# Optimization experiments

Measured on AMD Instinct MI355X. Metric: run time of the kernel, lower is better.

The kernel has to match this reference:

```python
import jax, jax.numpy as jnp
import numpy as np

COMMITMENT_COST = 0.25


def setup_inputs() -> dict:
    key = jax.random.key(0)
    k1, k2 = jax.random.split(key)
    B, S, D, K = 8, 4096, 256, 1024
    inputs = jax.random.normal(k1, (B, S, D), dtype=jnp.float32)
    attention_mask = jnp.ones((B, S), dtype=jnp.float32)
    codebook = jax.random.normal(k2, (K, D), dtype=jnp.float32)
    return {"inputs": inputs, "attention_mask": attention_mask, "codebook": codebook}


def reference(inputs, attention_mask, codebook):
    # Inference-mode forward of VectorQuantizer (no EMA update / init / revival).
    B, S, D = inputs.shape
    z = inputs.astype(jnp.float32).reshape(-1, D)          # (N, D)
    m = attention_mask.reshape(-1).astype(jnp.float32)     # (N,)

    cb = codebook.astype(jnp.float32)                      # (K, D)
    # squared L2 distances: ||z||^2 - 2 z e^T + ||e||^2
    dist = (jnp.sum(z * z, axis=-1, keepdims=True)
            - 2.0 * jnp.matmul(z, cb.T)
            + jnp.sum(cb * cb, axis=-1)[None, :])          # (N, K)
    idx = jnp.argmin(dist, axis=-1)                        # (N,)
    q = cb[idx]                                            # (N, D) codebook lookup

    n_valid = jnp.sum(m)
    # mse over valid tokens (elementwise mean, matching F.mse_loss on flat_valid)
    diff = z - jax.lax.stop_gradient(q)
    commitment = jnp.sum(m[:, None] * diff * diff) / (n_valid * D)
    vq_loss = COMMITMENT_COST * commitment

    # straight-through estimator; invalid positions zeroed (as in torch scatter)
    q_ste = z + jax.lax.stop_gradient(q - z)
    quantized = (q_ste * m[:, None]).reshape(B, S, D)
    indices = jnp.where(m > 0, idx, 0).reshape(B, S)
    return quantized, vq_loss, indices
```

## Files before the change

### kernel.cpp

```cpp
#include <hip/hip_runtime.h>
#include <cstdint>

typedef short bf16x8 __attribute__((ext_vector_type(8)));
typedef float f32x4  __attribute__((ext_vector_type(4)));

#define TOK    64
#define PITCH  264
#define HROWS  (64 * PITCH)
#define MAXC   32

__device__ __forceinline__ unsigned short f2bf(float f) {
  unsigned u = __float_as_uint(f);
  return (unsigned short)((u + 0x7FFFu + ((u >> 16) & 1u)) >> 16);
}
__device__ __forceinline__ uint4 pack8(float4 a, float4 b) {
  uint4 u;
  u.x = (unsigned)f2bf(a.x) | ((unsigned)f2bf(a.y) << 16);
  u.y = (unsigned)f2bf(a.z) | ((unsigned)f2bf(a.w) << 16);
  u.z = (unsigned)f2bf(b.x) | ((unsigned)f2bf(b.y) << 16);
  u.w = (unsigned)f2bf(b.z) | ((unsigned)f2bf(b.w) << 16);
  return u;
}

__global__ __launch_bounds__(256) void vq_prep(const float* __restrict__ cb,
                                               unsigned short* __restrict__ cb_bf,
                                               float* __restrict__ ee,
                                               float* __restrict__ acc2,
                                               int* __restrict__ done_ctr, int K) {
  if (blockIdx.x == 0 && threadIdx.x == 0) {
    acc2[0] = 0.f; acc2[1] = 0.f; *done_ctr = 0;
  }
  int wave = threadIdx.x >> 6, lane = threadIdx.x & 63;
  int k = blockIdx.x * 4 + wave;
  if (k >= K) return;
  float4 v = *reinterpret_cast<const float4*>(cb + (size_t)k * 256 + lane * 4);
  float s = v.x * v.x + v.y * v.y + v.z * v.z + v.w * v.w;
  #pragma unroll
  for (int off = 32; off; off >>= 1) s += __shfl_down(s, off, 64);
  ushort4 b;
  b.x = f2bf(v.x); b.y = f2bf(v.y); b.z = f2bf(v.z); b.w = f2bf(v.w);
  *reinterpret_cast<ushort4*>(cb_bf + (size_t)k * 256 + lane * 4) = b;
  if (lane == 0) ee[k] = s;
}

__global__ __launch_bounds__(256, 2) void vq_main(
    const float* __restrict__ z, const float* __restrict__ cb,
    const unsigned short* __restrict__ cb_bf, const float* __restrict__ ee,
    const float* __restrict__ mask,
    float* __restrict__ out_q, float* __restrict__ out_idx_f,
    float* __restrict__ out_loss, float* __restrict__ acc2,
    int* __restrict__ done_ctr, int nblocks, int K) {
  __shared__ __align__(16) unsigned short buf[128 * PITCH];
  __shared__ float ee_lds[1024];
  __shared__ float znorm[TOK];
  __shared__ int   ccnt[TOK];
  __shared__ unsigned short cand[TOK * MAXC];
  __shared__ float red[8];
  __shared__ bool  last;

  const int t = threadIdx.x;
  const int n0 = blockIdx.x * TOK;
  const int q16 = t & 15;

  ee_lds[t]       = ee[t];
  ee_lds[t + 256] = ee[t + 256];
  ee_lds[t + 512] = ee[t + 512];
  ee_lds[t + 768] = ee[t + 768];
  if (t < TOK) ccnt[t] = 0;

  #pragma unroll
  for (int pass = 0; pass < 4; ++pass) {
    int row = pass * 16 + (t >> 4);
    const float* zr = z + (size_t)(n0 + row) * 256;
    float ssq = 0.f;
    #pragma unroll
    for (int j = 0; j < 2; ++j) {
      float4 a = *reinterpret_cast<const float4*>(zr + q16 * 8 + j * 128);
      float4 b = *reinterpret_cast<const float4*>(zr + q16 * 8 + j * 128 + 4);
      ssq += a.x*a.x + a.y*a.y + a.z*a.z + a.w*a.w
           + b.x*b.x + b.y*b.y + b.z*b.z + b.w*b.w;
      *reinterpret_cast<uint4*>(&buf[row * PITCH + q16 * 8 + j * 128]) = pack8(a, b);
    }
    #pragma unroll
    for (int off = 1; off < 16; off <<= 1) ssq += __shfl_xor(ssq, off, 64);
    if (q16 == 0) znorm[row] = sqrtf(ssq);
  }
  __syncthreads();

  const int wv = t >> 6, lane = t & 63;
  const int p = wv & 1, kh = wv >> 1;
  const int quad = lane >> 4, l15 = lane & 15;
  bf16x8 afrag[2][8];
  float  znreg[2][4];
  #pragma unroll
  for (int s = 0; s < 2; ++s) {
    const unsigned short* za = &buf[(p * 32 + s * 16 + l15) * PITCH + quad * 8];
    #pragma unroll
    for (int kk = 0; kk < 8; ++kk)
      afrag[s][kk] = *reinterpret_cast<const bf16x8*>(za + kk * 32);
    #pragma unroll
    for (int r = 0; r < 4; ++r)
      znreg[s][r] = znorm[p * 32 + s * 16 + quad * 4 + r];
  }
  __syncthreads();

  float amin[2][4];
  #pragma unroll
  for (int s = 0; s < 2; ++s)
    #pragma unroll
    for (int r = 0; r < 4; ++r) amin[s][r] = 3.4e38f;

  const int tq = (p << 6) | lane;
  const int sq16 = tq & 15, srow = tq >> 4;
  unsigned short* qbuf = &buf[kh * HROWS];

  for (int lc = 0; lc < 8; ++lc) {
    const int kbase = kh * 512 + lc * 64;
    #pragma unroll
    for (int pass = 0; pass < 8; ++pass) {
      int row = pass * 8 + srow;
      const unsigned short* src = cb_bf + (size_t)(kbase + row) * 256;
      #pragma unroll
      for (int j = 0; j < 2; ++j) {
        uint4 v = *reinterpret_cast<const uint4*>(src + sq16 * 8 + j * 128);
        *reinterpret_cast<uint4*>(&qbuf[row * PITCH + sq16 * 8 + j * 128]) = v;
      }
    }
    __syncthreads();

    f32x4 acc[2][4];
    #pragma unroll
    for (int s = 0; s < 2; ++s)
      #pragma unroll
      for (int ct = 0; ct < 4; ++ct) acc[s][ct] = (f32x4){0.f, 0.f, 0.f, 0.f};
    #pragma unroll
    for (int kk = 0; kk < 8; ++kk) {
      bf16x8 b0 = *reinterpret_cast<const bf16x8*>(&qbuf[(l15)      * PITCH + quad * 8 + kk * 32]);
      bf16x8 b1 = *reinterpret_cast<const bf16x8*>(&qbuf[(16 + l15) * PITCH + quad * 8 + kk * 32]);
      bf16x8 b2 = *reinterpret_cast<const bf16x8*>(&qbuf[(32 + l15) * PITCH + quad * 8 + kk * 32]);
      bf16x8 b3 = *reinterpret_cast<const bf16x8*>(&qbuf[(48 + l15) * PITCH + quad * 8 + kk * 32]);
      acc[0][0] = __builtin_amdgcn_mfma_f32_16x16x32_bf16(afrag[0][kk], b0, acc[0][0], 0, 0, 0);
      acc[1][0] = __builtin_amdgcn_mfma_f32_16x16x32_bf16(afrag[1][kk], b0, acc[1][0], 0, 0, 0);
      acc[0][1] = __builtin_amdgcn_mfma_f32_16x16x32_bf16(afrag[0][kk], b1, acc[0][1], 0, 0, 0);
      acc[1][1] = __builtin_amdgcn_mfma_f32_16x16x32_bf16(afrag[1][kk], b1, acc[1][1], 0, 0, 0);
      acc[0][2] = __builtin_amdgcn_mfma_f32_16x16x32_bf16(afrag[0][kk], b2, acc[0][2], 0, 0, 0);
      acc[1][2] = __builtin_amdgcn_mfma_f32_16x16x32_bf16(afrag[1][kk], b2, acc[1][2], 0, 0, 0);
      acc[0][3] = __builtin_amdgcn_mfma_f32_16x16x32_bf16(afrag[0][kk], b3, acc[0][3], 0, 0, 0);
      acc[1][3] = __builtin_amdgcn_mfma_f32_16x16x32_bf16(afrag[1][kk], b3, acc[1][3], 0, 0, 0);
    }

    float e0 = ee_lds[kbase + l15],      e1 = ee_lds[kbase + 16 + l15];
    float e2 = ee_lds[kbase + 32 + l15], e3 = ee_lds[kbase + 48 + l15];
    float en0 = sqrtf(e0), en1 = sqrtf(e1), en2 = sqrtf(e2), en3 = sqrtf(e3);
    #pragma unroll
    for (int s = 0; s < 2; ++s) {
      #pragma unroll
      for (int r = 0; r < 4; ++r) {
        float d0 = e0 - 2.f * acc[s][0][r];
        float d1 = e1 - 2.f * acc[s][1][r];
        float d2 = e2 - 2.f * acc[s][2][r];
        float d3 = e3 - 2.f * acc[s][3][r];
        float w = fminf(fminf(d0, d1), fminf(d2, d3));
        #pragma unroll
        for (int off = 1; off < 16; off <<= 1) w = fminf(w, __shfl_xor(w, off, 64));
        float am = fminf(amin[s][r], w);
        amin[s][r] = am;
        int tok = p * 32 + s * 16 + quad * 4 + r;
        float zn = znreg[s][r];
        if (d0 <= am + 1.5f + 0.002f * zn * en0) {
          int sl = atomicAdd(&ccnt[tok], 1);
          if (sl < MAXC) cand[tok * MAXC + sl] = (unsigned short)(kbase + l15);
        }
        if (d1 <= am + 1.5f + 0.002f * zn * en1) {
          int sl = atomicAdd(&ccnt[tok], 1);
          if (sl < MAXC) cand[tok * MAXC + sl] = (unsigned short)(kbase + 16 + l15);
        }
        if (d2 <= am + 1.5f + 0.002f * zn * en2) {
          int sl = atomicAdd(&ccnt[tok], 1);
          if (sl < MAXC) cand[tok * MAXC + sl] = (unsigned short)(kbase + 32 + l15);
        }
        if (d3 <= am + 1.5f + 0.002f * zn * en3) {
          int sl = atomicAdd(&ccnt[tok], 1);
          if (sl < MAXC) cand[tok * MAXC + sl] = (unsigned short)(kbase + 48 + l15);
        }
      }
    }
    __syncthreads();
  }

  float lsum = 0.f, msum = 0.f;
  for (int it = 0; it < 16; ++it) {
    int tok = wv * 16 + it;
    int n = n0 + tok;
    float4 zv = *reinterpret_cast<const float4*>(z + (size_t)n * 256 + lane * 4);
    int cnt = ccnt[tok];
    float bs = 3.4e38f; int bk = 0;
    if (cnt > MAXC) {
      for (int k = 0; k < K; ++k) {
        float4 ev = *reinterpret_cast<const float4*>(cb + (size_t)k * 256 + lane * 4);
        float dp = zv.x * ev.x + zv.y * ev.y + zv.z * ev.z + zv.w * ev.w;
        #pragma unroll
        for (int off = 32; off; off >>= 1) dp += __shfl_xor(dp, off, 64);
        float s = ee_lds[k] - 2.f * dp;
        if (s < bs) { bs = s; bk = k; }
      }
    } else {
      for (int c = 0; c < cnt; ++c) {
        int k = cand[tok * MAXC + c];
        float4 ev = *reinterpret_cast<const float4*>(cb + (size_t)k * 256 + lane * 4);
        float dp = zv.x * ev.x + zv.y * ev.y + zv.z * ev.z + zv.w * ev.w;
        #pragma unroll
        for (int off = 32; off; off >>= 1) dp += __shfl_xor(dp, off, 64);
        float s = ee_lds[k] - 2.f * dp;
        if (s < bs || (s == bs && k < bk)) { bs = s; bk = k; }
      }
    }
    float m = mask[n];
    float4 qv = *reinterpret_cast<const float4*>(cb + (size_t)bk * 256 + lane * 4);
    float4 o; o.x = qv.x * m; o.y = qv.y * m; o.z = qv.z * m; o.w = qv.w * m;
    *reinterpret_cast<float4*>(out_q + (size_t)n * 256 + lane * 4) = o;
    float dx = zv.x - qv.x, dy = zv.y - qv.y, dz = zv.z - qv.z, dw = zv.w - qv.w;
    lsum = fmaf(m, dx * dx + dy * dy + dz * dz + dw * dw, lsum);
    if (lane == 0) {
      msum += m;
      out_idx_f[n] = (m > 0.f) ? (float)bk : 0.f;
    }
  }
  #pragma unroll
  for (int off = 32; off; off >>= 1) lsum += __shfl_down(lsum, off, 64);
  if (lane == 0) { red[wv] = lsum; red[4 + wv] = msum; }
  __syncthreads();
  if (t == 0) {
    atomicAdd(&acc2[0], red[0] + red[1] + red[2] + red[3]);
    atomicAdd(&acc2[1], red[4] + red[5] + red[6] + red[7]);
    __threadfence();
    int prev = atomicAdd(done_ctr, 1);
    last = (prev == nblocks - 1);
  }
  __syncthreads();
  if (last && t == 0) {
    float s  = atomicAdd(&acc2[0], 0.0f);
    float nv = atomicAdd(&acc2[1], 0.0f);
    out_loss[0] = (nv > 0.f) ? (0.25f * s / (nv * 256.0f)) : 0.0f;
  }
}

extern "C" void kernel_launch(void* const* d_in, const int* in_sizes, int n_in,
                              void* d_out, int out_size, void* d_ws, size_t ws_size,
                              hipStream_t stream) {
  const float* z    = (const float*)d_in[0];
  const float* mask = (const float*)d_in[1];
  const float* cb   = (const float*)d_in[2];
  const int N = in_sizes[1];
  const int D = 256;
  const int K = in_sizes[2] / D;

  float* wsf  = (float*)d_ws;
  float* acc2 = wsf;
  int*   dctr = (int*)(wsf + 2);
  float* ee   = wsf + 8;
  unsigned short* cb_bf = (unsigned short*)(ee + K);

  float* out_q     = (float*)d_out;
  float* out_loss  = out_q + (size_t)N * D;
  float* out_idx_f = out_loss + 1;

  vq_prep<<<(K + 3) / 4, 256, 0, stream>>>(cb, cb_bf, ee, acc2, dctr, K);
  vq_main<<<N / TOK, 256, 0, stream>>>(z, cb, cb_bf, ee, mask, out_q,
                                       out_idx_f, out_loss, acc2, dctr, N / TOK, K);
}
```

Baseline: 194.0 us.

## Double-buffer codebook chunks via direct global-to-LDS loads with XOR swizzle

Replaces the padded-pitch LDS layout with an XOR-swizzled layout and streams bf16 codebook chunks into a double buffer using global_load_lds, overlapping the next chunk's load with the current chunk's MFMA work. Work is also repartitioned so each wave owns 16 tokens across all 1024 codes instead of 32 tokens over half the codes. The aim is to hide global load latency and remove the register round-trip for staging. The trade-off is fewer MFMAs per B-fragment load, since there is no reuse across two token sub-tiles, and twice as many chunk iterations, each with its own barrier.

```diff
diff --git a/kernel.cpp b/kernel.cpp
--- a/kernel.cpp
+++ b/kernel.cpp
@@ -5,8 +5,9 @@
 typedef float f32x4  __attribute__((ext_vector_type(4)));
 
 #define TOK    64
-#define PITCH  264
-#define HROWS  (64 * PITCH)
+#define CH     64
+#define NCH    16
+#define BUFW   16384
 #define MAXC   32
 
 __device__ __forceinline__ unsigned short f2bf(float f) {
@@ -20,6 +21,11 @@
   u.z = (unsigned)f2bf(b.x) | ((unsigned)f2bf(b.y) << 16);
   u.w = (unsigned)f2bf(b.z) | ((unsigned)f2bf(b.w) << 16);
   return u;
+}
+__device__ __forceinline__ void gload16(const unsigned short* g, unsigned short* l) {
+  __builtin_amdgcn_global_load_lds(
+      (const __attribute__((address_space(1))) unsigned int*)(const void*)g,
+      (__attribute__((address_space(3))) unsigned int*)(void*)l, 16, 0, 0);
 }
 
 __global__ __launch_bounds__(256) void vq_prep(const float* __restrict__ cb,
@@ -50,7 +56,7 @@
     float* __restrict__ out_q, float* __restrict__ out_idx_f,
     float* __restrict__ out_loss, float* __restrict__ acc2,
     int* __restrict__ done_ctr, int nblocks, int K) {
-  __shared__ __align__(16) unsigned short buf[128 * PITCH];
+  __shared__ __align__(16) unsigned short sbuf[2 * BUFW];
   __shared__ float ee_lds[1024];
   __shared__ float znorm[TOK];
   __shared__ int   ccnt[TOK];
@@ -60,6 +66,8 @@
 
   const int t = threadIdx.x;
   const int n0 = blockIdx.x * TOK;
+  const int wv = t >> 6, lane = t & 63;
+  const int quad = lane >> 4, l15 = lane & 15;
   const int q16 = t & 15;
 
   ee_lds[t]       = ee[t];
@@ -75,11 +83,12 @@
     float ssq = 0.f;
     #pragma unroll
     for (int j = 0; j < 2; ++j) {
-      float4 a = *reinterpret_cast<const float4*>(zr + q16 * 8 + j * 128);
-      float4 b = *reinterpret_cast<const float4*>(zr + q16 * 8 + j * 128 + 4);
+      float4 a = *reinterpret_cast<const float4*>(zr + q16 * 16 + j * 8);
+      float4 b = *reinterpret_cast<const float4*>(zr + q16 * 16 + j * 8 + 4);
       ssq += a.x*a.x + a.y*a.y + a.z*a.z + a.w*a.w
            + b.x*b.x + b.y*b.y + b.z*b.z + b.w*b.w;
-      *reinterpret_cast<uint4*>(&buf[row * PITCH + q16 * 8 + j * 128]) = pack8(a, b);
+      int g = q16 * 2 + j;
+      *reinterpret_cast<uint4*>(&sbuf[row * 256 + ((g ^ (row & 7)) * 8)]) = pack8(a, b);
     }
     #pragma unroll
     for (int off = 1; off < 16; off <<= 1) ssq += __shfl_xor(ssq, off, 64);
@@ -87,104 +96,102 @@
   }
   __syncthreads();
 
-  const int wv = t >> 6, lane = t & 63;
-  const int p = wv & 1, kh = wv >> 1;
-  const int quad = lane >> 4, l15 = lane & 15;
-  bf16x8 afrag[2][8];
-  float  znreg[2][4];
-  #pragma unroll
-  for (int s = 0; s < 2; ++s) {
-    const unsigned short* za = &buf[(p * 32 + s * 16 + l15) * PITCH + quad * 8];
-    #pragma unroll
-    for (int kk = 0; kk < 8; ++kk)
-      afrag[s][kk] = *reinterpret_cast<const bf16x8*>(za + kk * 32);
+  bf16x8 afrag[8];
+  float  znreg[4];
+  {
+    int row = wv * 16 + l15;
+    #pragma unroll
+    for (int kk = 0; kk < 8; ++kk) {
+      int g = (quad + kk * 4) ^ (row & 7);
+      afrag[kk] = *reinterpret_cast<const bf16x8*>(&sbuf[row * 256 + g * 8]);
+    }
     #pragma unroll
     for (int r = 0; r < 4; ++r)
-      znreg[s][r] = znorm[p * 32 + s * 16 + quad * 4 + r];
-  }
-  __syncthreads();
-
-  float amin[2][4];
-  #pragma unroll
-  for (int s = 0; s < 2; ++s)
-    #pragma unroll
-    for (int r = 0; r < 4; ++r) amin[s][r] = 3.4e38f;
-
-  const int tq = (p << 6) | lane;
-  const int sq16 = tq & 15, srow = tq >> 4;
-  unsigned short* qbuf = &buf[kh * HROWS];
-
-  for (int lc = 0; lc < 8; ++lc) {
-    const int kbase = kh * 512 + lc * 64;
-    #pragma unroll
-    for (int pass = 0; pass < 8; ++pass) {
-      int row = pass * 8 + srow;
-      const unsigned short* src = cb_bf + (size_t)(kbase + row) * 256;
+      znreg[r] = znorm[wv * 16 + quad * 4 + r];
+  }
+  __syncthreads();
+
+  {
+    #pragma unroll
+    for (int i = 0; i < 8; ++i) {
+      int f = (wv * 8 + i) * 64 + lane;
+      int row = f >> 5, slot = f & 31;
+      gload16(cb_bf + (size_t)row * 256 + ((slot ^ (row & 7)) * 8),
+              &sbuf[(size_t)(wv * 512 + i * 64) * 8]);
+    }
+  }
+  asm volatile("s_waitcnt vmcnt(0)" ::: "memory");
+  __syncthreads();
+
+  float amin[4] = {3.4e38f, 3.4e38f, 3.4e38f, 3.4e38f};
+
+  for (int lc = 0; lc < NCH; ++lc) {
+    const int kbase = lc * CH;
+    unsigned short* cur = &sbuf[(lc & 1) * BUFW];
+    unsigned short* nxt = &sbuf[((lc + 1) & 1) * BUFW];
+    if (lc < NCH - 1) {
+      const unsigned short* base = cb_bf + (size_t)(kbase + CH) * 256;
       #pragma unroll
-      for (int j = 0; j < 2; ++j) {
-        uint4 v = *reinterpret_cast<const uint4*>(src + sq16 * 8 + j * 128);
-        *reinterpret_cast<uint4*>(&qbuf[row * PITCH + sq16 * 8 + j * 128]) = v;
-      }
-    }
-    __syncthreads();
-
-    f32x4 acc[2][4];
-    #pragma unroll
-    for (int s = 0; s < 2; ++s)
-      #pragma unroll
-      for (int ct = 0; ct < 4; ++ct) acc[s][ct] = (f32x4){0.f, 0.f, 0.f, 0.f};
+      for (int i = 0; i < 8; ++i) {
+        int f = (wv * 8 + i) * 64 + lane;
+        int row = f >> 5, slot = f & 31;
+        gload16(base + (size_t)row * 256 + ((slot ^ (row & 7)) * 8),
+                nxt + (size_t)(wv * 512 + i * 64) * 8);
+      }
+    }
+
+    f32x4 acc[4];
+    #pragma unroll
+    for (int ct = 0; ct < 4; ++ct) acc[ct] = (f32x4){0.f, 0.f, 0.f, 0.f};
+    __builtin_amdgcn_s_setprio(1);
     #pragma unroll
     for (int kk = 0; kk < 8; ++kk) {
-      bf16x8 b0 = *reinterpret_cast<const bf16x8*>(&qbuf[(l15)      * PITCH + quad * 8 + kk * 32]);
-      bf16x8 b1 = *reinterpret_cast<const bf16x8*>(&qbuf[(16 + l15) * PITCH + quad * 8 + kk * 32]);
-      bf16x8 b2 = *reinterpret_cast<const bf16x8*>(&qbuf[(32 + l15) * PITCH + quad * 8 + kk * 32]);
-      bf16x8 b3 = *reinterpret_cast<const bf16x8*>(&qbuf[(48 + l15) * PITCH + quad * 8 + kk * 32]);
-      acc[0][0] = __builtin_amdgcn_mfma_f32_16x16x32_bf16(afrag[0][kk], b0, acc[0][0], 0, 0, 0);
-      acc[1][0] = __builtin_amdgcn_mfma_f32_16x16x32_bf16(afrag[1][kk], b0, acc[1][0], 0, 0, 0);
-      acc[0][1] = __builtin_amdgcn_mfma_f32_16x16x32_bf16(afrag[0][kk], b1, acc[0][1], 0, 0, 0);
-      acc[1][1] = __builtin_amdgcn_mfma_f32_16x16x32_bf16(afrag[1][kk], b1, acc[1][1], 0, 0, 0);
-      acc[0][2] = __builtin_amdgcn_mfma_f32_16x16x32_bf16(afrag[0][kk], b2, acc[0][2], 0, 0, 0);
-      acc[1][2] = __builtin_amdgcn_mfma_f32_16x16x32_bf16(afrag[1][kk], b2, acc[1][2], 0, 0, 0);
-      acc[0][3] = __builtin_amdgcn_mfma_f32_16x16x32_bf16(afrag[0][kk], b3, acc[0][3], 0, 0, 0);
-      acc[1][3] = __builtin_amdgcn_mfma_f32_16x16x32_bf16(afrag[1][kk], b3, acc[1][3], 0, 0, 0);
-    }
+      int gx = quad + kk * 4;
+      bf16x8 b0 = *reinterpret_cast<const bf16x8*>(&cur[(l15)      * 256 + ((gx ^ ( l15       & 7)) * 8)]);
+      bf16x8 b1 = *reinterpret_cast<const bf16x8*>(&cur[(16 + l15) * 256 + ((gx ^ ((16 + l15) & 7)) * 8)]);
+      bf16x8 b2 = *reinterpret_cast<const bf16x8*>(&cur[(32 + l15) * 256 + ((gx ^ ((32 + l15) & 7)) * 8)]);
+      bf16x8 b3 = *reinterpret_cast<const bf16x8*>(&cur[(48 + l15) * 256 + ((gx ^ ((48 + l15) & 7)) * 8)]);
+      acc[0] = __builtin_amdgcn_mfma_f32_16x16x32_bf16(afrag[kk], b0, acc[0], 0, 0, 0);
+      acc[1] = __builtin_amdgcn_mfma_f32_16x16x32_bf16(afrag[kk], b1, acc[1], 0, 0, 0);
+      acc[2] = __builtin_amdgcn_mfma_f32_16x16x32_bf16(afrag[kk], b2, acc[2], 0, 0, 0);
+      acc[3] = __builtin_amdgcn_mfma_f32_16x16x32_bf16(afrag[kk], b3, acc[3], 0, 0, 0);
+    }
+    __builtin_amdgcn_s_setprio(0);
 
     float e0 = ee_lds[kbase + l15],      e1 = ee_lds[kbase + 16 + l15];
     float e2 = ee_lds[kbase + 32 + l15], e3 = ee_lds[kbase + 48 + l15];
     float en0 = sqrtf(e0), en1 = sqrtf(e1), en2 = sqrtf(e2), en3 = sqrtf(e3);
     #pragma unroll
-    for (int s = 0; s < 2; ++s) {
+    for (int r = 0; r < 4; ++r) {
+      float d0 = e0 - 2.f * acc[0][r];
+      float d1 = e1 - 2.f * acc[1][r];
+      float d2 = e2 - 2.f * acc[2][r];
+      float d3 = e3 - 2.f * acc[3][r];
+      float w = fminf(fminf(d0, d1), fminf(d2, d3));
       #pragma unroll
-      for (int r = 0; r < 4; ++r) {
-        float d0 = e0 - 2.f * acc[s][0][r];
-        float d1 = e1 - 2.f * acc[s][1][r];
-        float d2 = e2 - 2.f * acc[s][2][r];
-        float d3 = e3 - 2.f * acc[s][3][r];
-        float w = fminf(fminf(d0, d1), fminf(d2, d3));
-        #pragma unroll
-        for (int off = 1; off < 16; off <<= 1) w = fminf(w, __shfl_xor(w, off, 64));
-        float am = fminf(amin[s][r], w);
-        amin[s][r] = am;
-        int tok = p * 32 + s * 16 + quad * 4 + r;
-        float zn = znreg[s][r];
-        if (d0 <= am + 1.5f + 0.002f * zn * en0) {
-          int sl = atomicAdd(&ccnt[tok], 1);
-          if (sl < MAXC) cand[tok * MAXC + sl] = (unsigned short)(kbase + l15);
-        }
-        if (d1 <= am + 1.5f + 0.002f * zn * en1) {
-          int sl = atomicAdd(&ccnt[tok], 1);
-          if (sl < MAXC) cand[tok * MAXC + sl] = (unsigned short)(kbase + 16 + l15);
-        }
-        if (d2 <= am + 1.5f + 0.002f * zn * en2) {
-          int sl = atomicAdd(&ccnt[tok], 1);
-          if (sl < MAXC) cand[tok * MAXC + sl] = (unsigned short)(kbase + 32 + l15);
-        }
-        if (d3 <= am + 1.5f + 0.002f * zn * en3) {
-          int sl = atomicAdd(&ccnt[tok], 1);
-          if (sl < MAXC) cand[tok * MAXC + sl] = (unsigned short)(kbase + 48 + l15);
-        }
-      }
-    }
+      for (int off = 1; off < 16; off <<= 1) w = fminf(w, __shfl_xor(w, off, 64));
+      float am = fminf(amin[r], w);
+      amin[r] = am;
+      int tok = wv * 16 + quad * 4 + r;
+      float zn = znreg[r];
+      if (d0 <= am + 1.5f + 0.002f * zn * en0) {
+        int sl = atomicAdd(&ccnt[tok], 1);
+        if (sl < MAXC) cand[tok * MAXC + sl] = (unsigned short)(kbase + l15);
+      }
+      if (d1 <= am + 1.5f + 0.002f * zn * en1) {
+        int sl = atomicAdd(&ccnt[tok], 1);
+        if (sl < MAXC) cand[tok * MAXC + sl] = (unsigned short)(kbase + 16 + l15);
+      }
+      if (d2 <= am + 1.5f + 0.002f * zn * en2) {
+        int sl = atomicAdd(&ccnt[tok], 1);
+        if (sl < MAXC) cand[tok * MAXC + sl] = (unsigned short)(kbase + 32 + l15);
+      }
+      if (d3 <= am + 1.5f + 0.002f * zn * en3) {
+        int sl = atomicAdd(&ccnt[tok], 1);
+        if (sl < MAXC) cand[tok * MAXC + sl] = (unsigned short)(kbase + 48 + l15);
+      }
+    }
+    asm volatile("s_waitcnt vmcnt(0)" ::: "memory");
     __syncthreads();
   }
 
```

Result: faster. 182.8 us (-5.8%).
